# Kernel tuning notes

Hardware: AMD Instinct MI355X
Metric: run time of the kernel (lower is better)

The kernel has to match this reference:

```python
import jax, jax.numpy as jnp
import numpy as np

D_MODEL = 256
D_STATE = 16
D_CONV = 4
EXPAND = 2
D_INNER = EXPAND * D_MODEL
N = 65536


def setup_inputs() -> dict:
    key = jax.random.key(0)
    ks = jax.random.split(key, 16)
    s = lambda fan_in: 1.0 / np.sqrt(fan_in)
    inp = {
        'x': jax.random.normal(ks[0], (N, D_MODEL), jnp.float32),
        'guidance': jax.random.normal(ks[1], (N, 3), jnp.float32),
        'in_proj_w': jax.random.uniform(ks[2], (2 * D_INNER, D_MODEL), jnp.float32, -s(D_MODEL), s(D_MODEL)),
        'conv_w': jax.random.uniform(ks[3], (D_INNER, 1, D_CONV), jnp.float32, -s(D_CONV), s(D_CONV)),
        'conv_b': jax.random.uniform(ks[4], (D_INNER,), jnp.float32, -s(D_CONV), s(D_CONV)),
        'x_proj_w': jax.random.uniform(ks[5], (2 * D_STATE, D_INNER), jnp.float32, -s(D_INNER), s(D_INNER)),
        'dt_proj_w': jax.random.uniform(ks[6], (D_INNER, D_INNER), jnp.float32, -s(D_INNER), s(D_INNER)),
        'dt_proj_b': jax.random.uniform(ks[7], (D_INNER,), jnp.float32, -s(D_INNER), s(D_INNER)),
        'gg1_w': jax.random.uniform(ks[8], (D_INNER, 3), jnp.float32, -s(3), s(3)),
        'gg1_b': jax.random.uniform(ks[9], (D_INNER,), jnp.float32, -s(3), s(3)),
        'ln_g': jnp.ones((D_INNER,), jnp.float32),
        'ln_b': jnp.zeros((D_INNER,), jnp.float32),
        'gg2_w': jax.random.uniform(ks[10], (3 * D_INNER, D_INNER), jnp.float32, -s(D_INNER), s(D_INNER)),
        'gg2_b': jax.random.uniform(ks[11], (3 * D_INNER,), jnp.float32, -s(D_INNER), s(D_INNER)),
        'A_log': jnp.log(jnp.tile(jnp.arange(1, D_STATE + 1, dtype=jnp.float32), (D_INNER, 1))),
        'D': jnp.ones((D_INNER,), jnp.float32),
        'out_proj_w': jax.random.uniform(ks[12], (D_MODEL, D_INNER), jnp.float32, -s(D_INNER), s(D_INNER)),
    }
    return inp


def _layernorm(x, g, b, eps=1e-5):
    mu = jnp.mean(x, axis=-1, keepdims=True)
    var = jnp.var(x, axis=-1, keepdims=True)
    return (x - mu) * jax.lax.rsqrt(var + eps) * g + b


def _selective_scan(u, delta, A, B, C, Dp):
    # u, delta: [N, d_inner]; B, C: [N, d_state]; A: [d_inner, d_state]
    def step(h, inp):
        u_i, d_i, B_i, C_i = inp
        deltaA = jnp.exp(d_i[:, None] * A)                     # [d_inner, d_state]
        h = deltaA * h + (d_i[:, None] * B_i[None, :]) * u_i[:, None]
        y = jnp.sum(h * C_i[None, :], axis=-1) + Dp * u_i       # [d_inner]
        return h, y
    h0 = jnp.zeros((u.shape[1], A.shape[1]), u.dtype)
    _, ys = jax.lax.scan(step, h0, (u, delta, B, C))
    return ys                                                   # [N, d_inner]


def reference(x, guidance, in_proj_w, conv_w, conv_b, x_proj_w, dt_proj_w, dt_proj_b,
              gg1_w, gg1_b, ln_g, ln_b, gg2_w, gg2_b, A_log, D, out_proj_w):
    n = x.shape[0]
    xz = x @ in_proj_w.T                                        # [N, 2*d_inner]
    x_in, z = jnp.split(xz, 2, axis=-1)
    # depthwise causal conv1d over the voxel-sequence axis (pad left d_conv-1, crop to N)
    lhs = x_in.T[None]                                          # [1, d_inner, N]
    conv = jax.lax.conv_general_dilated(
        lhs, conv_w, window_strides=(1,), padding=[(D_CONV - 1, 0)],
        dimension_numbers=('NCH', 'OIH', 'NCH'), feature_group_count=D_INNER)
    x_in = conv[0].T + conv_b                                   # [N, d_inner]
    x_in = jax.nn.silu(x_in)
    # guidance gates
    g = _layernorm(guidance @ gg1_w.T + gg1_b, ln_g, ln_b)
    g = jax.nn.gelu(g, approximate=False)
    gates = g @ gg2_w.T + gg2_b                                 # [N, 3*d_inner]
    g_input, g_state, g_output = jnp.split(jax.nn.sigmoid(gates), 3, axis=-1)
    x_mod = x_in * g_input
    A = -jnp.exp(A_log)
    x_dbl = x_mod @ x_proj_w.T                                  # [N, 2*d_state]
    B, C = x_dbl[:, :D_STATE], x_dbl[:, D_STATE:]
    delta = jax.nn.softplus(x_mod @ dt_proj_w.T + dt_proj_b)
    y = _selective_scan(x_mod, delta, A, B, C, D)
    y = y * jax.nn.silu(z) * g_output
    return y @ out_proj_w.T                                     # [N, d_model]
```

## Files before the change

kernel.cpp:

```cpp
#include <hip/hip_runtime.h>
#include <math.h>

#define NTOK 65536
#define DMODEL 256
#define DI 512
#define DS 16
#define CHUNK 128
#define NCHUNK (NTOK / CHUNK)
#define QCH 128

typedef __bf16 bf16x8 __attribute__((ext_vector_type(8)));
typedef float  f32x4  __attribute__((ext_vector_type(4)));

__device__ __forceinline__ float sigf(float x) { return 1.0f / (1.0f + expf(-x)); }

__global__ __launch_bounds__(256) void wprep_kernel(
    const float* gg2_w, unsigned short* Wg)
{
    int p = blockIdx.x * 256 + threadIdx.x;
    int lg = p & 3;
    int c  = (p >> 2) & 511;
    int hl = (p >> 11) & 1;
    int kc = (p >> 12) & 15;
    int gm = p >> 16;
// ... 3 lines not shown
#pragma unroll
    for (int j = 0; j < 8; j++) {
        float x = src[j];
        __bf16 h = (__bf16)x;
        union { __bf16 b; unsigned short us; } cv;
        if (hl) cv.b = (__bf16)(x - (float)h); else cv.b = h;
        outv.u[j] = cv.us;
    }
    *(float4*)(Wg + (size_t)p * 8) = outv.f;
}

__global__ __launch_bounds__(256) void wprep_inproj(
    const float* in_proj_w, unsigned short* Wg2)
{
    int p = blockIdx.x * 256 + threadIdx.x;
    int lg = p & 3;
    int c  = (p >> 2) & 511;
    int hl = (p >> 11) & 1;
    int kc = (p >> 12) & 7;
    int gm = p >> 15;
    const float* src = in_proj_w + (size_t)(gm * 512 + c) * 256 + kc * 32 + lg * 8;
    union { unsigned short u[8]; float4 f; } outv;
#pragma unroll
    for (int j = 0; j < 8; j++) {
        float x = src[j];
        __bf16 h = (__bf16)x;
        union { __bf16 b; unsigned short us; } cv;
        if (hl) cv.b = (__bf16)(x - (float)h); else cv.b = h;
        outv.u[j] = cv.us;
    }
    *(float4*)(Wg2 + (size_t)p * 8) = outv.f;
}

__global__ __launch_bounds__(256) void wprep_dt(
    const float* dt_proj_w, unsigned short* Wdt)
{
    int p = blockIdx.x * 256 + threadIdx.x;
    int lg = p & 3;
    int c  = (p >> 2) & 127;
    int hl = (p >> 9) & 1;
    int kc = (p >> 10) & 15;
    int q  = p >> 14;
    const float* src = dt_proj_w + (size_t)(q * 128 + c) * 512 + kc * 32 + lg * 8;
    union { unsigned short u[8]; float4 f; } outv;
#pragma unroll
    for (int j = 0; j < 8; j++) {
        float x = src[j];
        __bf16 h = (__bf16)x;
        union { __bf16 b; unsigned short us; } cv;
        if (hl) cv.b = (__bf16)(x - (float)h); else cv.b = h;
        outv.u[j] = cv.us;
    }
    *(float4*)(Wdt + (size_t)p * 8) = outv.f;
}

__global__ __launch_bounds__(256) void wprep_out(
    const float* out_proj_w, unsigned short* Wout)
{
    int p = blockIdx.x * 256 + threadIdx.x;
    int lg = p & 3;
    int c  = (p >> 2) & 255;
    int hl = (p >> 10) & 1;
    int kc = p >> 11;
    const float* src = out_proj_w + (size_t)c * 512 + kc * 32 + lg * 8;
    union { unsigned short u[8]; float4 f; } outv;
#pragma unroll
    for (int j = 0; j < 8; j++) {
        float x = src[j];
        __bf16 h = (__bf16)x;
        union { __bf16 b; unsigned short us; } cv;
        if (hl) cv.b = (__bf16)(x - (float)h); else cv.b = h;
        outv.u[j] = cv.us;
    }
    *(float4*)(Wout + (size_t)p * 8) = outv.f;
}

#define MFMA_CHUNK(NFM, KC, WH, WL)                                           \
    _Pragma("unroll")                                                         \
    for (int fm = 0; fm < NFM; fm++) {                                        \
        int t = (fm < 4) ? (fm * 16 + lr) : (64 + lr);                        \
        int pidx = (t * 32 + (((KC) * 4 + lg) ^ (t & 7))) * 8;                \
        bf16x8 ah = *(const bf16x8*)&AhL[pidx];                               \
        bf16x8 al = *(const bf16x8*)&AlL[pidx];                               \
        _Pragma("unroll")                                                     \
        for (int fn = 0; fn < 4; fn++) {                                      \
            acc[fm][fn] = __builtin_amdgcn_mfma_f32_16x16x32_bf16(ah, WH[fn], acc[fm][fn], 0, 0, 0); \
            acc[fm][fn] = __builtin_amdgcn_mfma_f32_16x16x32_bf16(ah, WL[fn], acc[fm][fn], 0, 0, 0); \
            acc[fm][fn] = __builtin_amdgcn_mfma_f32_16x16x32_bf16(al, WH[fn], acc[fm][fn], 0, 0, 0); \
        }                                                                     \
    }

__global__ __launch_bounds__(512, 2) void in_conv_mfma(
    const float* x, const unsigned short* Wg2, const float* conv_w,
    const float* conv_b, float* P1, float* P2)
{
    __shared__ __align__(16) unsigned short smem[2 * 80 * 256];
    unsigned short* AhL = smem;
    unsigned short* AlL = smem + 80 * 256;
    float* xs = (float*)smem;

    const int tid = threadIdx.x;
    const int row0 = blockIdx.x * 64;
    const int l  = tid & 63;
    const int wn = tid >> 6;
    const int lr = l & 15;
    const int lg = l >> 4;
// ... 75 lines not shown
                acc[fm][fn] = (f32x4){0.f, 0.f, 0.f, 0.f};
        bf16x8 whA[4], wlA[4], whB[4], wlB[4];
        loadW(0, 0, whA, wlA);
#pragma unroll
        for (int kc = 0; kc < 8; kc += 2) {
            loadW(0, kc + 1, whB, wlB);
            MFMA_CHUNK(5, kc, whA, wlA)
            if (kc + 2 < 8) loadW(0, kc + 2, whA, wlA);
            MFMA_CHUNK(5, kc + 1, whB, wlB)
        }

        __syncthreads();
        float* xsw = xs + wn * (68 * 33);
        const int c_local = l & 31;
        const int rbase = (l >> 5) * 32;
#pragma unroll
        for (int h = 0; h < 2; h++) {
            if (h) __syncthreads();
#pragma unroll
            for (int fm = 0; fm < 5; fm++)
#pragma unroll
                for (int ff = 0; ff < 2; ff++) {
                    int fn = h * 2 + ff;
#pragma unroll
                    for (int q = 0; q < 4; q++) {
                        if (fm < 4) {
                            int rr = 4 + fm * 16 + lg * 4 + q;
                            xsw[rr * 33 + ff * 16 + lr] = acc[fm][fn][q];
                        } else if (lg == 0) {
                            xsw[q * 33 + ff * 16 + lr] = acc[fm][fn][q];
                        }
                    }
                }
            asm volatile("s_waitcnt lgkmcnt(0)" ::: "memory");
            int cg = wn * 64 + h * 32 + c_local;
            float w0 = conv_w[cg * 4 + 0], w1 = conv_w[cg * 4 + 1];
            float w2 = conv_w[cg * 4 + 2], w3 = conv_w[cg * 4 + 3];
            float cb = conv_b[cg];
            float s0 = xsw[(rbase + 1) * 33 + c_local];
            float s1 = xsw[(rbase + 2) * 33 + c_local];
            float s2 = xsw[(rbase + 3) * 33 + c_local];
#pragma unroll
            for (int i = 0; i < 32; i++) {
                float s3 = xsw[(rbase + 4 + i) * 33 + c_local];
                float cv = cb + w0 * s0 + w1 * s1 + w2 * s2 + w3 * s3;
                cv = cv * sigf(cv);
                P1[(size_t)(row0 + rbase + i) * 512 + cg] = cv;
                s0 = s1; s1 = s2; s2 = s3;
            }
        }
    }
}

__global__ __launch_bounds__(512, 2) void gates_mfma_kernel(
    const float* guidance, const float* gg1_w, const float* gg1_b,
    const float* ln_g, const float* ln_b,
    const unsigned short* Wg, const float* gg2_b,
    float* P1, float* P2)
{
    __shared__ unsigned short AhL[64 * 512];
    __shared__ unsigned short AlL[64 * 512];
    __shared__ float red_s[64][9], red_q[64][9];

    const int tid = threadIdx.x;
    const int tok = tid & 63;
    const int o   = tid >> 6;
    const int row0 = blockIdx.x * 64;

    float g0 = guidance[(size_t)(row0 + tok) * 3 + 0];
    float g1 = guidance[(size_t)(row0 + tok) * 3 + 1];
    float g2 = guidance[(size_t)(row0 + tok) * 3 + 2];
    float v[64];
    float sum = 0.f, sumsq = 0.f;
#pragma unroll
    for (int m = 0; m < 8; m++)
#pragma unroll
        for (int jj = 0; jj < 8; jj++) {
            int d = m * 64 + o * 8 + jj;
            float t = gg1_w[d * 3 + 0] * g0 + gg1_w[d * 3 + 1] * g1 +
                      gg1_w[d * 3 + 2] * g2 + gg1_b[d];
            v[m * 8 + jj] = t;
            sum += t; sumsq += t * t;
        }
    red_s[tok][o] = sum; red_q[tok][o] = sumsq;
    __syncthreads();
    sum = 0.f; sumsq = 0.f;
#pragma unroll
    for (int oo = 0; oo < 8; oo++) { sum += red_s[tok][oo]; sumsq += red_q[tok][oo]; }
    float mu = sum * (1.f / 512.f);
    float var = fmaxf(sumsq * (1.f / 512.f) - mu * mu, 0.f);
    float rstd = 1.f / sqrtf(var + 1e-5f);
#pragma unroll
    for (int m = 0; m < 8; m++) {
        bf16x8 hoct, loct;
#pragma unroll
        for (int jj = 0; jj < 8; jj++) {
            int d = m * 64 + o * 8 + jj;
            float t = (v[m * 8 + jj] - mu) * rstd * ln_g[d] + ln_b[d];
            t = 0.5f * t * (1.f + erff(t * 0.70710678118654752440f));
            __bf16 h = (__bf16)t;
            hoct[jj] = h;
            loct[jj] = (__bf16)(t - (float)h);
        }
        int pidx = ((tok * 64 + (m * 8 + o)) ^ (tok & 7)) * 8;
        *(bf16x8*)&AhL[pidx] = hoct;
        *(bf16x8*)&AlL[pidx] = loct;
    }
    __syncthreads();

    const int l  = tid & 63;
    const int wn = tid >> 6;
    const int lr = l & 15;
    const int lg = l >> 4;

    for (int gm = 0; gm < 2; gm++) {
        f32x4 acc[4][4];
#pragma unroll
        for (int fm = 0; fm < 4; fm++)
#pragma unroll
            for (int fn = 0; fn < 4; fn++)
                acc[fm][fn] = (f32x4){0.f, 0.f, 0.f, 0.f};

        bf16x8 whA[4], wlA[4], whB[4], wlB[4];

        auto loadW = [&](int kc, bf16x8 (&wh)[4], bf16x8 (&wl)[4]) {
            const unsigned short* bh = Wg + (size_t)(((gm * 16 + kc) * 2 + 0) * 2048) * 8;
            const unsigned short* bl = Wg + (size_t)(((gm * 16 + kc) * 2 + 1) * 2048) * 8;
            int pk = (wn * 64 + lr) * 4 + lg;
#pragma unroll
            for (int fn = 0; fn < 4; fn++) {
                wh[fn] = *(const bf16x8*)(bh + (size_t)(pk + fn * 64) * 8);
                wl[fn] = *(const bf16x8*)(bl + (size_t)(pk + fn * 64) * 8);
            }
        };
        auto doChunk = [&](int kc, const bf16x8 (&wh)[4], const bf16x8 (&wl)[4]) {
#pragma unroll
            for (int fm = 0; fm < 4; fm++) {
                int t = fm * 16 + lr;
                int pidx = ((t * 64 + kc * 4 + lg) ^ (lr & 7)) * 8;
                bf16x8 ah = *(const bf16x8*)&AhL[pidx];
                bf16x8 al = *(const bf16x8*)&AlL[pidx];
#pragma unroll
                for (int fn = 0; fn < 4; fn++) {
                    acc[fm][fn] = __builtin_amdgcn_mfma_f32_16x16x32_bf16(
                        ah, wh[fn], acc[fm][fn], 0, 0, 0);
                    acc[fm][fn] = __builtin_amdgcn_mfma_f32_16x16x32_bf16(
                        ah, wl[fn], acc[fm][fn], 0, 0, 0);
                    acc[fm][fn] = __builtin_amdgcn_mfma_f32_16x16x32_bf16(
                        al, wh[fn], acc[fm][fn], 0, 0, 0);
                }
            }
        };

        loadW(0, whA, wlA);
        for (int kc = 0; kc < 16; kc += 2) {
            loadW(kc + 1, whB, wlB);
            doChunk(kc, whA, wlA);
            if (kc + 2 < 16) loadW(kc + 2, whA, wlA);
            doChunk(kc + 1, whB, wlB);
        }

        float* P = gm ? P2 : P1;
        const float* bias = gg2_b + gm * 1024;
#pragma unroll
        for (int fm = 0; fm < 4; fm++)
#pragma unroll
            for (int fn = 0; fn < 4; fn++) {
                int col = wn * 64 + fn * 16 + lr;
                float b = bias[col];
#pragma unroll
                for (int q = 0; q < 4; q++) {
                    int r = row0 + fm * 16 + lg * 4 + q;
                    size_t idx = (size_t)r * 512 + col;
                    P[idx] *= sigf(acc[fm][fn][q] + b);
                }
            }
    }
}

__global__ __launch_bounds__(512, 2) void dtp_mfma(
    const float* A, const unsigned short* Wdt, const float* bias,
    int dbase, float* delta_q)
{
    __shared__ __align__(16) unsigned short AhL[64 * 512];
    __shared__ __align__(16) unsigned short AlL[64 * 512];
    const int tid = threadIdx.x;
    const int row0 = blockIdx.x * 64;

    for (int i = tid; i < 64 * 64; i += 512) {
        int t = i >> 6, k8 = i & 63;
        const float* src = A + (size_t)(row0 + t) * 512 + k8 * 8;
        float4 a0 = *(const float4*)src, a1 = *(const float4*)(src + 4);
        float xv[8] = {a0.x, a0.y, a0.z, a0.w, a1.x, a1.y, a1.z, a1.w};
        bf16x8 ho, lo;
#pragma unroll
        for (int j = 0; j < 8; j++) {
            __bf16 hh = (__bf16)xv[j];
            ho[j] = hh;
            lo[j] = (__bf16)(xv[j] - (float)hh);
        }
        int pidx = (t * 64 + (k8 ^ (t & 7))) * 8;
        *(bf16x8*)&AhL[pidx] = ho;
        *(bf16x8*)&AlL[pidx] = lo;
    }
    __syncthreads();

    const int l  = tid & 63;
    const int wv = tid >> 6;
    const int wr = wv >> 2;
    const int wc = wv & 3;
    const int lr = l & 15;
    const int lg = l >> 4;
    const unsigned short* Wq = Wdt + (size_t)(dbase >> 7) * 16384 * 8;

    f32x4 acc[2][2];
#pragma unroll
    for (int fm = 0; fm < 2; fm++)
#pragma unroll
        for (int fn = 0; fn < 2; fn++)
            acc[fm][fn] = (f32x4){0.f, 0.f, 0.f, 0.f};

    bf16x8 whA[2], wlA[2], whB[2], wlB[2];
    auto loadW = [&](int kc, bf16x8 (&wh)[2], bf16x8 (&wl)[2]) {
        const unsigned short* bh = Wq + (size_t)((kc * 2 + 0) * 512) * 8;
        const unsigned short* bl = Wq + (size_t)((kc * 2 + 1) * 512) * 8;
        int pk = (wc * 32 + lr) * 4 + lg;
#pragma unroll
        for (int fn = 0; fn < 2; fn++) {
            wh[fn] = *(const bf16x8*)(bh + (size_t)(pk + fn * 64) * 8);
            wl[fn] = *(const bf16x8*)(bl + (size_t)(pk + fn * 64) * 8);
        }
    };
    auto doChunk = [&](int kc, const bf16x8 (&wh)[2], const bf16x8 (&wl)[2]) {
#pragma unroll
        for (int fm = 0; fm < 2; fm++) {
            int t = wr * 32 + fm * 16 + lr;
            int pidx = (t * 64 + ((kc * 4 + lg) ^ (t & 7))) * 8;
            bf16x8 ah = *(const bf16x8*)&AhL[pidx];
            bf16x8 al = *(const bf16x8*)&AlL[pidx];
#pragma unroll
            for (int fn = 0; fn < 2; fn++) {
                acc[fm][fn] = __builtin_amdgcn_mfma_f32_16x16x32_bf16(
                    ah, wh[fn], acc[fm][fn], 0, 0, 0);
                acc[fm][fn] = __builtin_amdgcn_mfma_f32_16x16x32_bf16(
                    ah, wl[fn], acc[fm][fn], 0, 0, 0);
                acc[fm][fn] = __builtin_amdgcn_mfma_f32_16x16x32_bf16(
                    al, wh[fn], acc[fm][fn], 0, 0, 0);
            }
        }
    };

    loadW(0, whA, wlA);
    for (int kc = 0; kc < 16; kc += 2) {
        loadW(kc + 1, whB, wlB);
        doChunk(kc, whA, wlA);
        if (kc + 2 < 16) loadW(kc + 2, whA, wlA);
        doChunk(kc + 1, whB, wlB);
    }

#pragma unroll
    for (int fm = 0; fm < 2; fm++)
#pragma unroll
        for (int fn = 0; fn < 2; fn++) {
            int col = wc * 32 + fn * 16 + lr;
            float b = bias[dbase + col];
#pragma unroll
            for (int q = 0; q < 4; q++) {
                int r = row0 + wr * 32 + fm * 16 + lg * 4 + q;
                float s = acc[fm][fn][q] + b;
                delta_q[(size_t)r * 128 + col] =
                    fmaxf(s, 0.f) + log1pf(expf(-fabsf(s)));
            }
        }
}

__global__ __launch_bounds__(512, 2) void outp_mfma(
    const float* A, const unsigned short* Wout, float* out)
{
    __shared__ __align__(16) unsigned short AhL[64 * 512];
    __shared__ __align__(16) unsigned short AlL[64 * 512];
    const int tid = threadIdx.x;
    const int row0 = blockIdx.x * 64;

    for (int i = tid; i < 64 * 64; i += 512) {
        int t = i >> 6, k8 = i & 63;
        const float* src = A + (size_t)(row0 + t) * 512 + k8 * 8;
        float4 a0 = *(const float4*)src, a1 = *(const float4*)(src + 4);
        float xv[8] = {a0.x, a0.y, a0.z, a0.w, a1.x, a1.y, a1.z, a1.w};
        bf16x8 ho, lo;
#pragma unroll
        for (int j = 0; j < 8; j++) {
            __bf16 hh = (__bf16)xv[j];
            ho[j] = hh;
            lo[j] = (__bf16)(xv[j] - (float)hh);
        }
        int pidx = (t * 64 + (k8 ^ (t & 7))) * 8;
        *(bf16x8*)&AhL[pidx] = ho;
        *(bf16x8*)&AlL[pidx] = lo;
    }
    __syncthreads();

    const int l  = tid & 63;
    const int wv = tid >> 6;
    const int wr = wv >> 2;
    const int wc = wv & 3;
    const int lr = l & 15;
    const int lg = l >> 4;

    f32x4 acc[2][4];
#pragma unroll
    for (int fm = 0; fm < 2; fm++)
#pragma unroll
        for (int fn = 0; fn < 4; fn++)
            acc[fm][fn] = (f32x4){0.f, 0.f, 0.f, 0.f};

    bf16x8 whA[4], wlA[4], whB[4], wlB[4];
    auto loadW = [&](int kc, bf16x8 (&wh)[4], bf16x8 (&wl)[4]) {
        const unsigned short* bh = Wout + (size_t)((kc * 2 + 0) * 1024) * 8;
        const unsigned short* bl = Wout + (size_t)((kc * 2 + 1) * 1024) * 8;
        int pk = (wc * 64 + lr) * 4 + lg;
#pragma unroll
        for (int fn = 0; fn < 4; fn++) {
            wh[fn] = *(const bf16x8*)(bh + (size_t)(pk + fn * 64) * 8);
            wl[fn] = *(const bf16x8*)(bl + (size_t)(pk + fn * 64) * 8);
        }
    };
    auto doChunk = [&](int kc, const bf16x8 (&wh)[4], const bf16x8 (&wl)[4]) {
#pragma unroll
        for (int fm = 0; fm < 2; fm++) {
            int t = wr * 32 + fm * 16 + lr;
            int pidx = (t * 64 + ((kc * 4 + lg) ^ (t & 7))) * 8;
            bf16x8 ah = *(const bf16x8*)&AhL[pidx];
            bf16x8 al = *(const bf16x8*)&AlL[pidx];
#pragma unroll
            for (int fn = 0; fn < 4; fn++) {
                acc[fm][fn] = __builtin_amdgcn_mfma_f32_16x16x32_bf16(
                    ah, wh[fn], acc[fm][fn], 0, 0, 0);
                acc[fm][fn] = __builtin_amdgcn_mfma_f32_16x16x32_bf16(
                    ah, wl[fn], acc[fm][fn], 0, 0, 0);
                acc[fm][fn] = __builtin_amdgcn_mfma_f32_16x16x32_bf16(
                    al, wh[fn], acc[fm][fn], 0, 0, 0);
            }
        }
    };

    loadW(0, whA, wlA);
    for (int kc = 0; kc < 16; kc += 2) {
        loadW(kc + 1, whB, wlB);
        doChunk(kc, whA, wlA);
        if (kc + 2 < 16) loadW(kc + 2, whA, wlA);
        doChunk(kc + 1, whB, wlB);
    }

#pragma unroll
    for (int fm = 0; fm < 2; fm++)
#pragma unroll
        for (int fn = 0; fn < 4; fn++) {
            int col = wc * 64 + fn * 16 + lr;
#pragma unroll
            for (int q = 0; q < 4; q++) {
                int r = row0 + wr * 32 + fm * 16 + lg * 4 + q;
                out[(size_t)r * 256 + col] = acc[fm][fn][q];
            }
        }
}

__global__ __launch_bounds__(256) void gemm_nt32(
    const float* A, const float* W, float* out0, int K, int ldo)
{
    __shared__ float As[16][65];
    __shared__ float Ws[16][33];
    const int tid = threadIdx.x;
    const int row0 = blockIdx.x * 64;
    const int tr = (tid / 16) * 4;
    const int tc = (tid % 16) * 2;
    float acc[4][2];
#pragma unroll
    for (int i = 0; i < 4; i++) { acc[i][0] = 0.f; acc[i][1] = 0.f; }
    for (int k0 = 0; k0 < K; k0 += 16) {
        __syncthreads();
        for (int i = tid; i < 64 * 16; i += 256) {
            int m = i / 16, k = i % 16;
            As[k][m] = A[(size_t)(row0 + m) * K + k0 + k];
        }
        for (int i = tid; i < 32 * 16; i += 256) {
            int n = i / 16, k = i % 16;
            Ws[k][n] = W[(size_t)n * K + k0 + k];
        }
        __syncthreads();
#pragma unroll
        for (int kk = 0; kk < 16; kk++) {
            float a[4], b[2];
#pragma unroll
            for (int i = 0; i < 4; i++) a[i] = As[kk][tr + i];
            b[0] = Ws[kk][tc]; b[1] = Ws[kk][tc + 1];
#pragma unroll
            for (int i = 0; i < 4; i++) { acc[i][0] += a[i] * b[0]; acc[i][1] += a[i] * b[1]; }
        }
    }
#pragma unroll
    for (int i = 0; i < 4; i++) {
        int r = row0 + tr + i;
        out0[(size_t)r * ldo + tc] = acc[i][0];
        out0[(size_t)r * ldo + tc + 1] = acc[i][1];
    }
}

__global__ __launch_bounds__(256) void scan_pass1(
    const float* delta_q, const float* u_full, const float* xdbl,
    const float* A_log, int dbase, float* h_end, float* Ssum)
{
    int c = blockIdx.x;
    int tid = threadIdx.x;
    int dl = tid >> 1;
    int sh = (tid & 1) * 8;
    int d = dbase + dl;
    float As[8];
#pragma unroll
    for (int s = 0; s < 8; s++) As[s] = -expf(A_log[d * 16 + sh + s]);
    float h[8];
#pragma unroll
    for (int s = 0; s < 8; s++) h[s] = 0.f;
    float S = 0.f;
    __shared__ float Bs[CHUNK][17];
    int tbase = c * CHUNK;
    for (int i = tid; i < CHUNK * 16; i += 256) {
        int r = i >> 4, s = i & 15;
        Bs[r][s] = xdbl[(size_t)(tbase + r) * 32 + s];
    }
    __syncthreads();
    for (int tl = 0; tl < CHUNK; tl++) {
        size_t t = (size_t)tbase + tl;
        float de = delta_q[t * QCH + dl];
        float uu = u_full[t * DI + d];
        float du = de * uu;
        S += de;
#pragma unroll
        for (int s = 0; s < 8; s++)
            h[s] = __expf(de * As[s]) * h[s] + du * Bs[tl][sh + s];
    }
    size_t base = ((size_t)c * QCH + dl) * 16 + sh;
#pragma unroll
    for (int s = 0; s < 8; s++) h_end[base + s] = h[s];
    if ((tid & 1) == 0) Ssum[(size_t)c * QCH + dl] = S;
}

#define GRP 16
#define NGRP (NCHUNK / GRP)

__global__ __launch_bounds__(256) void scan_pass2a(
    const float* h_end, const float* Ssum, const float* A_log, int dbase,
    float* Pagg, float* Hagg)
{
    int idx = blockIdx.x * 256 + threadIdx.x;
    int g = blockIdx.y;
    int dl = idx >> 4;
    float As = -expf(A_log[(dbase + dl) * 16 + (idx & 15)]);
    float P = 1.f, H = 0.f;
// ... 65 lines not shown
        float de = delta_q[t * QCH + dl];
        float uu = u_full[t * DI + d];
        float du = de * uu;
        float y = 0.f;
#pragma unroll
        for (int s = 0; s < 8; s++) {
            h[s] = __expf(de * As[s]) * h[s] + du * Bs[tl][sh + s];
            y += h[s] * Cs[tl][sh + s];
        }
        y += __shfl_xor(y, 1);
        if ((tid & 1) == 0)
            wg_ymod[t * DI + d] = (y + Dd * uu) * wg_ymod[t * DI + d];
    }
}

extern "C" void kernel_launch(void* const* d_in, const int* in_sizes, int n_in,
                              void* d_out, int out_size, void* d_ws, size_t ws_size,
                              hipStream_t stream)
{
    const float* x         = (const float*)d_in[0];
    const float* guidance  = (const float*)d_in[1];
    const float* in_proj_w = (const float*)d_in[2];
    const float* conv_w    = (const float*)d_in[3];
    const float* conv_b    = (const float*)d_in[4];
    const float* x_proj_w  = (const float*)d_in[5];
    const float* dt_proj_w = (const float*)d_in[6];
    const float* dt_proj_b = (const float*)d_in[7];
    const float* gg1_w     = (const float*)d_in[8];
    const float* gg1_b     = (const float*)d_in[9];
    const float* ln_g      = (const float*)d_in[10];
    const float* ln_b      = (const float*)d_in[11];
    const float* gg2_w     = (const float*)d_in[12];
    const float* gg2_b     = (const float*)d_in[13];
    const float* A_log     = (const float*)d_in[14];
    const float* Dp        = (const float*)d_in[15];
    const float* out_proj_w= (const float*)d_in[16];
    float* out = (float*)d_out;

    float* P1 = (float*)d_ws;
    float* P2 = P1 + (size_t)NTOK * DI;

    float* ob      = (float*)d_out;
    float* delta_q = ob;
    float* xdbl    = ob + (size_t)NTOK * QCH;
    float* h_end   = ob + (size_t)NTOK * (QCH + 32);
    float* Ssum    = h_end + (size_t)NCHUNK * QCH * DS;
    float* initS   = Ssum + (size_t)NCHUNK * QCH;
    unsigned short* Wg  = (unsigned short*)(initS + (size_t)NCHUNK * QCH * DS);
    unsigned short* Wg2 = Wg  + (size_t)131072 * 8;
    unsigned short* Wdt = Wg2 + (size_t)65536 * 8;
    float* Pagg  = (float*)(Wdt + (size_t)65536 * 8);
    float* Hagg  = Pagg + NGRP * 2048;
    float* Ginit = Hagg + NGRP * 2048;
    unsigned short* Wout = (unsigned short*)P1;

    wprep_kernel<<<512, 256, 0, stream>>>(gg2_w, Wg);
    wprep_inproj<<<256, 256, 0, stream>>>(in_proj_w, Wg2);
    wprep_dt<<<256, 256, 0, stream>>>(dt_proj_w, Wdt);
    in_conv_mfma<<<NTOK / 64, 512, 0, stream>>>(
        x, Wg2, conv_w, conv_b, P1, P2);
    gates_mfma_kernel<<<NTOK / 64, 512, 0, stream>>>(
        guidance, gg1_w, gg1_b, ln_g, ln_b, Wg, gg2_b, P1, P2);
    gemm_nt32<<<NTOK / 64, 256, 0, stream>>>(P1, x_proj_w, xdbl, DI, 32);
    for (int q = 0; q < 4; q++) {
        int dbase = q * QCH;
        dtp_mfma<<<NTOK / 64, 512, 0, stream>>>(
            P1, Wdt, dt_proj_b, dbase, delta_q);
        scan_pass1<<<NCHUNK, 256, 0, stream>>>(
            delta_q, P1, xdbl, A_log, dbase, h_end, Ssum);
        scan_pass2a<<<dim3(8, NGRP), 256, 0, stream>>>(
            h_end, Ssum, A_log, dbase, Pagg, Hagg);
        scan_pass2b<<<8, 256, 0, stream>>>(Pagg, Hagg, Ginit);
        scan_pass2c<<<dim3(8, NGRP), 256, 0, stream>>>(
            h_end, Ssum, A_log, dbase, Ginit, initS);
        scan_pass3<<<NCHUNK, 256, 0, stream>>>(
            delta_q, P1, xdbl, A_log, dbase, initS, Dp, P2);
    }
    wprep_out<<<128, 256, 0, stream>>>(out_proj_w, Wout);
    outp_mfma<<<NTOK / 64, 512, 0, stream>>>(P2, Wout, out);
}
```

Baseline: 1.795 ms.

## Halve LDS tiles via K-split staging and raise occupancy in MFMA GEMM kernels

The gates, dt-proj and out-proj MFMA kernels now stage the split-bf16 activation tile in two K halves of 256, halving shared memory per block, and launch bounds go from 2 to 4 blocks per CU. The gates kernel also moves its two output groups onto a second grid dimension instead of looping, and recomputes the LayerNorm input instead of holding 64 values in registers. The weight-load double buffering is dropped in favour of plain per-chunk loads, leaning on the higher occupancy to hide latency. The costs are an extra barrier per block, duplicated LayerNorm/GELU work in the gates kernel, and tighter register limits that could cause spills.

```diff
diff --git a/kernel.cpp b/kernel.cpp
--- a/kernel.cpp
+++ b/kernel.cpp
@@ -260,25 +260,25 @@
     }
 }
 
-__global__ __launch_bounds__(512, 2) void gates_mfma_kernel(
+__global__ __launch_bounds__(512, 4) void gates_mfma_kernel(
     const float* guidance, const float* gg1_w, const float* gg1_b,
     const float* ln_g, const float* ln_b,
     const unsigned short* Wg, const float* gg2_b,
     float* P1, float* P2)
 {
-    __shared__ unsigned short AhL[64 * 512];
-    __shared__ unsigned short AlL[64 * 512];
+    __shared__ __align__(16) unsigned short AhL[64 * 256];
+    __shared__ __align__(16) unsigned short AlL[64 * 256];
     __shared__ float red_s[64][9], red_q[64][9];
 
     const int tid = threadIdx.x;
     const int tok = tid & 63;
     const int o   = tid >> 6;
     const int row0 = blockIdx.x * 64;
+    const int gm  = blockIdx.y;
 
     float g0 = guidance[(size_t)(row0 + tok) * 3 + 0];
     float g1 = guidance[(size_t)(row0 + tok) * 3 + 1];
     float g2 = guidance[(size_t)(row0 + tok) * 3 + 2];
-    float v[64];
     float sum = 0.f, sumsq = 0.f;
 #pragma unroll
     for (int m = 0; m < 8; m++)
@@ -287,7 +287,6 @@
             int d = m * 64 + o * 8 + jj;
             float t = gg1_w[d * 3 + 0] * g0 + gg1_w[d * 3 + 1] * g1 +
                       gg1_w[d * 3 + 2] * g2 + gg1_b[d];
-            v[m * 8 + jj] = t;
             sum += t; sumsq += t * t;
         }
     red_s[tok][o] = sum; red_q[tok][o] = sumsq;
@@ -298,54 +297,59 @@
     float mu = sum * (1.f / 512.f);
     float var = fmaxf(sumsq * (1.f / 512.f) - mu * mu, 0.f);
     float rstd = 1.f / sqrtf(var + 1e-5f);
-#pragma unroll
-    for (int m = 0; m < 8; m++) {
-        bf16x8 hoct, loct;
-#pragma unroll
-        for (int jj = 0; jj < 8; jj++) {
-            int d = m * 64 + o * 8 + jj;
-            float t = (v[m * 8 + jj] - mu) * rstd * ln_g[d] + ln_b[d];
-            t = 0.5f * t * (1.f + erff(t * 0.70710678118654752440f));
-            __bf16 h = (__bf16)t;
-            hoct[jj] = h;
-            loct[jj] = (__bf16)(t - (float)h);
-        }
-        int pidx = ((tok * 64 + (m * 8 + o)) ^ (tok & 7)) * 8;
-        *(bf16x8*)&AhL[pidx] = hoct;
-        *(bf16x8*)&AlL[pidx] = loct;
-    }
-    __syncthreads();
 
     const int l  = tid & 63;
     const int wn = tid >> 6;
     const int lr = l & 15;
     const int lg = l >> 4;
 
-    for (int gm = 0; gm < 2; gm++) {
-        f32x4 acc[4][4];
-#pragma unroll
-        for (int fm = 0; fm < 4; fm++)
-#pragma unroll
-            for (int fn = 0; fn < 4; fn++)
-                acc[fm][fn] = (f32x4){0.f, 0.f, 0.f, 0.f};
-
-        bf16x8 whA[4], wlA[4], whB[4], wlB[4];
-
-        auto loadW = [&](int kc, bf16x8 (&wh)[4], bf16x8 (&wl)[4]) {
-            const unsigned short* bh = Wg + (size_t)(((gm * 16 + kc) * 2 + 0) * 2048) * 8;
-            const unsigned short* bl = Wg + (size_t)(((gm * 16 + kc) * 2 + 1) * 2048) * 8;
-            int pk = (wn * 64 + lr) * 4 + lg;
-#pragma unroll
-            for (int fn = 0; fn < 4; fn++) {
-                wh[fn] = *(const bf16x8*)(bh + (size_t)(pk + fn * 64) * 8);
-                wl[fn] = *(const bf16x8*)(bl + (size_t)(pk + fn * 64) * 8);
-            }
-        };
-        auto doChunk = [&](int kc, const bf16x8 (&wh)[4], const bf16x8 (&wl)[4]) {
+    f32x4 acc[4][4];
+#pragma unroll
+    for (int fm = 0; fm < 4; fm++)
+#pragma unroll
+        for (int fn = 0; fn < 4; fn++)
+            acc[fm][fn] = (f32x4){0.f, 0.f, 0.f, 0.f};
+
+    for (int kh = 0; kh < 2; kh++) {
+        __syncthreads();
+#pragma unroll
+        for (int mm = 0; mm < 4; mm++) {
+            int m = kh * 4 + mm;
+            bf16x8 hoct, loct;
+#pragma unroll
+            for (int jj = 0; jj < 8; jj++) {
+                int d = m * 64 + o * 8 + jj;
+                float t = gg1_w[d * 3 + 0] * g0 + gg1_w[d * 3 + 1] * g1 +
+                          gg1_w[d * 3 + 2] * g2 + gg1_b[d];
+                t = (t - mu) * rstd * ln_g[d] + ln_b[d];
+                t = 0.5f * t * (1.f + erff(t * 0.70710678118654752440f));
+                __bf16 h = (__bf16)t;
+                hoct[jj] = h;
+                loct[jj] = (__bf16)(t - (float)h);
+            }
+            int k8l = mm * 8 + o;
+            int pidx = (tok * 32 + (k8l ^ (tok & 7))) * 8;
+            *(bf16x8*)&AhL[pidx] = hoct;
+            *(bf16x8*)&AlL[pidx] = loct;
+        }
+        __syncthreads();
+        for (int kc = 0; kc < 8; kc++) {
+            bf16x8 wh[4], wl[4];
+            {
+                int kcg = kh * 8 + kc;
+                const unsigned short* bh = Wg + (size_t)(((gm * 16 + kcg) * 2 + 0) * 2048) * 8;
+                const unsigned short* bl = Wg + (size_t)(((gm * 16 + kcg) * 2 + 1) * 2048) * 8;
+                int pk = (wn * 64 + lr) * 4 + lg;
+#pragma unroll
+                for (int fn = 0; fn < 4; fn++) {
+                    wh[fn] = *(const bf16x8*)(bh + (size_t)(pk + fn * 64) * 8);
+                    wl[fn] = *(const bf16x8*)(bl + (size_t)(pk + fn * 64) * 8);
+                }
+            }
 #pragma unroll
             for (int fm = 0; fm < 4; fm++) {
                 int t = fm * 16 + lr;
-                int pidx = ((t * 64 + kc * 4 + lg) ^ (lr & 7)) * 8;
+                int pidx = (t * 32 + ((kc * 4 + lg) ^ (t & 7))) * 8;
                 bf16x8 ah = *(const bf16x8*)&AhL[pidx];
                 bf16x8 al = *(const bf16x8*)&AlL[pidx];
 #pragma unroll
@@ -358,60 +362,34 @@
                         al, wh[fn], acc[fm][fn], 0, 0, 0);
                 }
             }
-        };
-
-        loadW(0, whA, wlA);
-        for (int kc = 0; kc < 16; kc += 2) {
-            loadW(kc + 1, whB, wlB);
-            doChunk(kc, whA, wlA);
-            if (kc + 2 < 16) loadW(kc + 2, whA, wlA);
-            doChunk(kc + 1, whB, wlB);
-        }
-
-        float* P = gm ? P2 : P1;
-        const float* bias = gg2_b + gm * 1024;
-#pragma unroll
-        for (int fm = 0; fm < 4; fm++)
-#pragma unroll
-            for (int fn = 0; fn < 4; fn++) {
-                int col = wn * 64 + fn * 16 + lr;
-                float b = bias[col];
-#pragma unroll
-                for (int q = 0; q < 4; q++) {
-                    int r = row0 + fm * 16 + lg * 4 + q;
-                    size_t idx = (size_t)r * 512 + col;
-                    P[idx] *= sigf(acc[fm][fn][q] + b);
-                }
-            }
-    }
-}
-
-__global__ __launch_bounds__(512, 2) void dtp_mfma(
+        }
+    }
+
+    float* P = gm ? P2 : P1;
+    const float* bias = gg2_b + gm * 1024;
+#pragma unroll
+    for (int fm = 0; fm < 4; fm++)
+#pragma unroll
+        for (int fn = 0; fn < 4; fn++) {
+            int col = wn * 64 + fn * 16 + lr;
+            float b = bias[col];
+#pragma unroll
+            for (int q = 0; q < 4; q++) {
+                int r = row0 + fm * 16 + lg * 4 + q;
+                size_t idx = (size_t)r * 512 + col;
+                P[idx] *= sigf(acc[fm][fn][q] + b);
+            }
+        }
+}
+
+__global__ __launch_bounds__(512, 4) void dtp_mfma(
     const float* A, const unsigned short* Wdt, const float* bias,
     int dbase, float* delta_q)
 {
-    __shared__ __align__(16) unsigned short AhL[64 * 512];
-    __shared__ __align__(16) unsigned short AlL[64 * 512];
+    __shared__ __align__(16) unsigned short AhL[64 * 256];
+    __shared__ __align__(16) unsigned short AlL[64 * 256];
     const int tid = threadIdx.x;
     const int row0 = blockIdx.x * 64;
-
-    for (int i = tid; i < 64 * 64; i += 512) {
-        int t = i >> 6, k8 = i & 63;
-        const float* src = A + (size_t)(row0 + t) * 512 + k8 * 8;
-        float4 a0 = *(const float4*)src, a1 = *(const float4*)(src + 4);
-        float xv[8] = {a0.x, a0.y, a0.z, a0.w, a1.x, a1.y, a1.z, a1.w};
-        bf16x8 ho, lo;
-#pragma unroll
-        for (int j = 0; j < 8; j++) {
-            __bf16 hh = (__bf16)xv[j];
-            ho[j] = hh;
-            lo[j] = (__bf16)(xv[j] - (float)hh);
-        }
-        int pidx = (t * 64 + (k8 ^ (t & 7))) * 8;
-        *(bf16x8*)&AhL[pidx] = ho;
-        *(bf16x8*)&AlL[pidx] = lo;
-    }
-    __syncthreads();
 
     const int l  = tid & 63;
     const int wv = tid >> 6;
@@ -428,42 +406,55 @@
         for (int fn = 0; fn < 2; fn++)
             acc[fm][fn] = (f32x4){0.f, 0.f, 0.f, 0.f};
 
-    bf16x8 whA[2], wlA[2], whB[2], wlB[2];
-    auto loadW = [&](int kc, bf16x8 (&wh)[2], bf16x8 (&wl)[2]) {
-        const unsigned short* bh = Wq + (size_t)((kc * 2 + 0) * 512) * 8;
-        const unsigned short* bl = Wq + (size_t)((kc * 2 + 1) * 512) * 8;
-        int pk = (wc * 32 + lr) * 4 + lg;
-#pragma unroll
-        for (int fn = 0; fn < 2; fn++) {
-            wh[fn] = *(const bf16x8*)(bh + (size_t)(pk + fn * 64) * 8);
-            wl[fn] = *(const bf16x8*)(bl + (size_t)(pk + fn * 64) * 8);
-        }
-    };
-    auto doChunk = [&](int kc, const bf16x8 (&wh)[2], const bf16x8 (&wl)[2]) {
-#pragma unroll
-        for (int fm = 0; fm < 2; fm++) {
-            int t = wr * 32 + fm * 16 + lr;
-            int pidx = (t * 64 + ((kc * 4 + lg) ^ (t & 7))) * 8;
-            bf16x8 ah = *(const bf16x8*)&AhL[pidx];
-            bf16x8 al = *(const bf16x8*)&AlL[pidx];
-#pragma unroll
-            for (int fn = 0; fn < 2; fn++) {
-                acc[fm][fn] = __builtin_amdgcn_mfma_f32_16x16x32_bf16(
-                    ah, wh[fn], acc[fm][fn], 0, 0, 0);
-                acc[fm][fn] = __builtin_amdgcn_mfma_f32_16x16x32_bf16(
-                    ah, wl[fn], acc[fm][fn], 0, 0, 0);
-                acc[fm][fn] = __builtin_amdgcn_mfma_f32_16x16x32_bf16(
-                    al, wh[fn], acc[fm][fn], 0, 0, 0);
-            }
-        }
-    };
-
-    loadW(0, whA, wlA);
-    for (int kc = 0; kc < 16; kc += 2) {
-        loadW(kc + 1, whB, wlB);
-        doChunk(kc, whA, wlA);
-        if (kc + 2 < 16) loadW(kc + 2, whA, wlA);
-        doChunk(kc + 1, whB, wlB);
+    for (int kh = 0; kh < 2; kh++) {
+        if (kh) __syncthreads();
+        for (int i = tid; i < 64 * 32; i += 512) {
+            int t = i >> 5, k8 = i & 31;
+            const float* src = A + (size_t)(row0 + t) * 512 + kh * 256 + k8 * 8;
+            float4 a0 = *(const float4*)src, a1 = *(const float4*)(src + 4);
+            float xv[8] = {a0.x, a0.y, a0.z, a0.w, a1.x, a1.y, a1.z, a1.w};
+            bf16x8 ho, lo;
+#pragma unroll
+            for (int j = 0; j < 8; j++) {
+                __bf16 hh = (__bf16)xv[j];
+                ho[j] = hh;
+                lo[j] = (__bf16)(xv[j] - (float)hh);
+            }
+            int pidx = (t * 32 + (k8 ^ (t & 7))) * 8;
+            *(bf16x8*)&AhL[pidx] = ho;
+            *(bf16x8*)&AlL[pidx] = lo;
+        }
+        __syncthreads();
+        for (int kc = 0; kc < 8; kc++) {
+            bf16x8 wh[2], wl[2];
+            {
+                int kcg = kh * 8 + kc;
+                const unsigned short* bh = Wq + (size_t)((kcg * 2 + 0) * 512) * 8;
+                const unsigned short* bl = Wq + (size_t)((kcg * 2 + 1) * 512) * 8;
+                int pk = (wc * 32 + lr) * 4 + lg;
+#pragma unroll
+                for (int fn = 0; fn < 2; fn++) {
+                    wh[fn] = *(const bf16x8*)(bh + (size_t)(pk + fn * 64) * 8);
+                    wl[fn] = *(const bf16x8*)(bl + (size_t)(pk + fn * 64) * 8);
+                }
+            }
+#pragma unroll
+            for (int fm = 0; fm < 2; fm++) {
+                int t = wr * 32 + fm * 16 + lr;
+                int pidx = (t * 32 + ((kc * 4 + lg) ^ (t & 7))) * 8;
+                bf16x8 ah = *(const bf16x8*)&AhL[pidx];
+                bf16x8 al = *(const bf16x8*)&AlL[pidx];
+#pragma unroll
+                for (int fn = 0; fn < 2; fn++) {
+                    acc[fm][fn] = __builtin_amdgcn_mfma_f32_16x16x32_bf16(
+                        ah, wh[fn], acc[fm][fn], 0, 0, 0);
+                    acc[fm][fn] = __builtin_amdgcn_mfma_f32_16x16x32_bf16(
+                        ah, wl[fn], acc[fm][fn], 0, 0, 0);
+                    acc[fm][fn] = __builtin_amdgcn_mfma_f32_16x16x32_bf16(
+                        al, wh[fn], acc[fm][fn], 0, 0, 0);
+                }
+            }
+        }
     }
 
 #pragma unroll
@@ -482,31 +473,13 @@
         }
 }
 
-__global__ __launch_bounds__(512, 2) void outp_mfma(
+__global__ __launch_bounds__(512, 4) void outp_mfma(
     const float* A, const unsigned short* Wout, float* out)
 {
-    __shared__ __align__(16) unsigned short AhL[64 * 512];
-    __shared__ __align__(16) unsigned short AlL[64 * 512];
+    __shared__ __align__(16) unsigned short AhL[64 * 256];
+    __shared__ __align__(16) unsigned short AlL[64 * 256];
     const int tid = threadIdx.x;
     const int row0 = blockIdx.x * 64;
-
-    for (int i = tid; i < 64 * 64; i += 512) {
-        int t = i >> 6, k8 = i & 63;
-        const float* src = A + (size_t)(row0 + t) * 512 + k8 * 8;
-        float4 a0 = *(const float4*)src, a1 = *(const float4*)(src + 4);
-        float xv[8] = {a0.x, a0.y, a0.z, a0.w, a1.x, a1.y, a1.z, a1.w};
-        bf16x8 ho, lo;
-#pragma unroll
-        for (int j = 0; j < 8; j++) {
-            __bf16 hh = (__bf16)xv[j];
-            ho[j] = hh;
-            lo[j] = (__bf16)(xv[j] - (float)hh);
-        }
-        int pidx = (t * 64 + (k8 ^ (t & 7))) * 8;
-        *(bf16x8*)&AhL[pidx] = ho;
-        *(bf16x8*)&AlL[pidx] = lo;
-    }
-    __syncthreads();
 
     const int l  = tid & 63;
     const int wv = tid >> 6;
@@ -522,42 +495,55 @@
         for (int fn = 0; fn < 4; fn++)
             acc[fm][fn] = (f32x4){0.f, 0.f, 0.f, 0.f};
 
-    bf16x8 whA[4], wlA[4], whB[4], wlB[4];
-    auto loadW = [&](int kc, bf16x8 (&wh)[4], bf16x8 (&wl)[4]) {
-        const unsigned short* bh = Wout + (size_t)((kc * 2 + 0) * 1024) * 8;
-        const unsigned short* bl = Wout + (size_t)((kc * 2 + 1) * 1024) * 8;
-        int pk = (wc * 64 + lr) * 4 + lg;
-#pragma unroll
-        for (int fn = 0; fn < 4; fn++) {
-            wh[fn] = *(const bf16x8*)(bh + (size_t)(pk + fn * 64) * 8);
-            wl[fn] = *(const bf16x8*)(bl + (size_t)(pk + fn * 64) * 8);
-        }
-    };
-    auto doChunk = [&](int kc, const bf16x8 (&wh)[4], const bf16x8 (&wl)[4]) {
-#pragma unroll
-        for (int fm = 0; fm < 2; fm++) {
-            int t = wr * 32 + fm * 16 + lr;
-            int pidx = (t * 64 + ((kc * 4 + lg) ^ (t & 7))) * 8;
-            bf16x8 ah = *(const bf16x8*)&AhL[pidx];
-            bf16x8 al = *(const bf16x8*)&AlL[pidx];
-#pragma unroll
-            for (int fn = 0; fn < 4; fn++) {
-                acc[fm][fn] = __builtin_amdgcn_mfma_f32_16x16x32_bf16(
-                    ah, wh[fn], acc[fm][fn], 0, 0, 0);
-                acc[fm][fn] = __builtin_amdgcn_mfma_f32_16x16x32_bf16(
-                    ah, wl[fn], acc[fm][fn], 0, 0, 0);
-                acc[fm][fn] = __builtin_amdgcn_mfma_f32_16x16x32_bf16(
-                    al, wh[fn], acc[fm][fn], 0, 0, 0);
-            }
-        }
-    };
-
-    loadW(0, whA, wlA);
-    for (int kc = 0; kc < 16; kc += 2) {
-        loadW(kc + 1, whB, wlB);
-        doChunk(kc, whA, wlA);
-        if (kc + 2 < 16) loadW(kc + 2, whA, wlA);
-        doChunk(kc + 1, whB, wlB);
+    for (int kh = 0; kh < 2; kh++) {
+        if (kh) __syncthreads();
+        for (int i = tid; i < 64 * 32; i += 512) {
+            int t = i >> 5, k8 = i & 31;
+            const float* src = A + (size_t)(row0 + t) * 512 + kh * 256 + k8 * 8;
+            float4 a0 = *(const float4*)src, a1 = *(const float4*)(src + 4);
+            float xv[8] = {a0.x, a0.y, a0.z, a0.w, a1.x, a1.y, a1.z, a1.w};
+            bf16x8 ho, lo;
+#pragma unroll
+            for (int j = 0; j < 8; j++) {
+                __bf16 hh = (__bf16)xv[j];
+                ho[j] = hh;
+                lo[j] = (__bf16)(xv[j] - (float)hh);
+            }
+            int pidx = (t * 32 + (k8 ^ (t & 7))) * 8;
+            *(bf16x8*)&AhL[pidx] = ho;
+            *(bf16x8*)&AlL[pidx] = lo;
+        }
+        __syncthreads();
+        for (int kc = 0; kc < 8; kc++) {
+            bf16x8 wh[4], wl[4];
+            {
+                int kcg = kh * 8 + kc;
+                const unsigned short* bh = Wout + (size_t)((kcg * 2 + 0) * 1024) * 8;
+                const unsigned short* bl = Wout + (size_t)((kcg * 2 + 1) * 1024) * 8;
+                int pk = (wc * 64 + lr) * 4 + lg;
+#pragma unroll
+                for (int fn = 0; fn < 4; fn++) {
+                    wh[fn] = *(const bf16x8*)(bh + (size_t)(pk + fn * 64) * 8);
+                    wl[fn] = *(const bf16x8*)(bl + (size_t)(pk + fn * 64) * 8);
+                }
+            }
+#pragma unroll
+            for (int fm = 0; fm < 2; fm++) {
+                int t = wr * 32 + fm * 16 + lr;
+                int pidx = (t * 32 + ((kc * 4 + lg) ^ (t & 7))) * 8;
+                bf16x8 ah = *(const bf16x8*)&AhL[pidx];
+                bf16x8 al = *(const bf16x8*)&AlL[pidx];
+#pragma unroll
+                for (int fn = 0; fn < 4; fn++) {
+                    acc[fm][fn] = __builtin_amdgcn_mfma_f32_16x16x32_bf16(
+                        ah, wh[fn], acc[fm][fn], 0, 0, 0);
+                    acc[fm][fn] = __builtin_amdgcn_mfma_f32_16x16x32_bf16(
+                        ah, wl[fn], acc[fm][fn], 0, 0, 0);
+                    acc[fm][fn] = __builtin_amdgcn_mfma_f32_16x16x32_bf16(
+                        al, wh[fn], acc[fm][fn], 0, 0, 0);
+                }
+            }
+        }
     }
 
 #pragma unroll
@@ -790,7 +776,7 @@
     wprep_dt<<<256, 256, 0, stream>>>(dt_proj_w, Wdt);
     in_conv_mfma<<<NTOK / 64, 512, 0, stream>>>(
         x, Wg2, conv_w, conv_b, P1, P2);
-    gates_mfma_kernel<<<NTOK / 64, 512, 0, stream>>>(
+    gates_mfma_kernel<<<dim3(NTOK / 64, 2), 512, 0, stream>>>(
         guidance, gg1_w, gg1_b, ln_g, ln_b, Wg, gg2_b, P1, P2);
     gemm_nt32<<<NTOK / 64, 256, 0, stream>>>(P1, x_proj_w, xdbl, DI, 32);
     for (int q = 0; q < 4; q++) {
```

Result: slower. 1.922 ms (+7.1%).

## Fuse x_proj GEMM into first dt_proj MFMA pass and triple-buffer gate weights

Applied to the files above, without the earlier changes.

Removes the separate FP32 SIMT gemm_nt32 kernel for x_proj. Its weights are now pre-split into bf16 hi/lo and the product is computed with MFMA inside the first dt_proj kernel launch, reusing the A tiles already staged in shared memory. Only waves with wc<2 do the extra MFMAs, which adds some imbalance within that launch. Separately, the gates kernel now keeps three register buffers of weight chunks in a fully unrolled loop, which raises register pressure.

```diff
diff --git a/kernel.cpp b/kernel.cpp
--- a/kernel.cpp
+++ b/kernel.cpp
@@ -79,6 +79,27 @@
         outv.u[j] = cv.us;
     }
     *(float4*)(Wdt + (size_t)p * 8) = outv.f;
+}
+
+__global__ __launch_bounds__(256) void wprep_xp(
+    const float* x_proj_w, unsigned short* Wxp)
+{
+    int p = blockIdx.x * 256 + threadIdx.x;
+    int lg = p & 3;
+    int c  = (p >> 2) & 31;
+    int hl = (p >> 7) & 1;
+    int kc = p >> 8;
+    const float* src = x_proj_w + (size_t)c * 512 + kc * 32 + lg * 8;
+    union { unsigned short u[8]; float4 f; } outv;
+#pragma unroll
+    for (int j = 0; j < 8; j++) {
+        float x = src[j];
+        __bf16 h = (__bf16)x;
+        union { __bf16 b; unsigned short us; } cv;
+        if (hl) cv.b = (__bf16)(x - (float)h); else cv.b = h;
+        outv.u[j] = cv.us;
+    }
+    *(float4*)(Wxp + (size_t)p * 8) = outv.f;
 }
 
 __global__ __launch_bounds__(256) void wprep_out(
@@ -329,7 +350,7 @@
             for (int fn = 0; fn < 4; fn++)
                 acc[fm][fn] = (f32x4){0.f, 0.f, 0.f, 0.f};
 
-        bf16x8 whA[4], wlA[4], whB[4], wlB[4];
+        bf16x8 whB3[3][4], wlB3[3][4];
 
         auto loadW = [&](int kc, bf16x8 (&wh)[4], bf16x8 (&wl)[4]) {
             const unsigned short* bh = Wg + (size_t)(((gm * 16 + kc) * 2 + 0) * 2048) * 8;
@@ -360,12 +381,12 @@
             }
         };
 
-        loadW(0, whA, wlA);
-        for (int kc = 0; kc < 16; kc += 2) {
-            loadW(kc + 1, whB, wlB);
-            doChunk(kc, whA, wlA);
-            if (kc + 2 < 16) loadW(kc + 2, whA, wlA);
-            doChunk(kc + 1, whB, wlB);
+        loadW(0, whB3[0], wlB3[0]);
+        loadW(1, whB3[1], wlB3[1]);
+#pragma unroll
+        for (int i = 0; i < 16; i++) {
+            if (i + 2 < 16) loadW(i + 2, whB3[(i + 2) % 3], wlB3[(i + 2) % 3]);
+            doChunk(i, whB3[i % 3], wlB3[i % 3]);
         }
 
         float* P = gm ? P2 : P1;
@@ -386,9 +407,10 @@
     }
 }
 
+template <bool XP>
 __global__ __launch_bounds__(512, 2) void dtp_mfma(
-    const float* A, const unsigned short* Wdt, const float* bias,
-    int dbase, float* delta_q)
+    const float* A, const unsigned short* Wdt, const unsigned short* Wxp,
+    const float* bias, int dbase, float* delta_q, float* xdbl)
 {
     __shared__ __align__(16) unsigned short AhL[64 * 512];
     __shared__ __align__(16) unsigned short AlL[64 * 512];
@@ -420,6 +442,7 @@
     const int lr = l & 15;
     const int lg = l >> 4;
     const unsigned short* Wq = Wdt + (size_t)(dbase >> 7) * 16384 * 8;
+    const bool doXP = XP && (wc < 2);
 
     f32x4 acc[2][2];
 #pragma unroll
@@ -427,9 +450,14 @@
 #pragma unroll
         for (int fn = 0; fn < 2; fn++)
             acc[fm][fn] = (f32x4){0.f, 0.f, 0.f, 0.f};
+    f32x4 axp[2];
+    axp[0] = (f32x4){0.f, 0.f, 0.f, 0.f};
+    axp[1] = (f32x4){0.f, 0.f, 0.f, 0.f};
 
     bf16x8 whA[2], wlA[2], whB[2], wlB[2];
-    auto loadW = [&](int kc, bf16x8 (&wh)[2], bf16x8 (&wl)[2]) {
+    bf16x8 xwA, xlA, xwB, xlB;
+    auto loadW = [&](int kc, bf16x8 (&wh)[2], bf16x8 (&wl)[2],
+                     bf16x8& xw, bf16x8& xl) {
         const unsigned short* bh = Wq + (size_t)((kc * 2 + 0) * 512) * 8;
         const unsigned short* bl = Wq + (size_t)((kc * 2 + 1) * 512) * 8;
         int pk = (wc * 32 + lr) * 4 + lg;
@@ -438,8 +466,16 @@
             wh[fn] = *(const bf16x8*)(bh + (size_t)(pk + fn * 64) * 8);
             wl[fn] = *(const bf16x8*)(bl + (size_t)(pk + fn * 64) * 8);
         }
+        if (doXP) {
+            const unsigned short* xh = Wxp + (size_t)((kc * 2 + 0) * 128) * 8;
+            const unsigned short* xlo = Wxp + (size_t)((kc * 2 + 1) * 128) * 8;
+            int pkx = (wc * 16 + lr) * 4 + lg;
+            xw = *(const bf16x8*)(xh + (size_t)pkx * 8);
+            xl = *(const bf16x8*)(xlo + (size_t)pkx * 8);
+        }
     };
-    auto doChunk = [&](int kc, const bf16x8 (&wh)[2], const bf16x8 (&wl)[2]) {
+    auto doChunk = [&](int kc, const bf16x8 (&wh)[2], const bf16x8 (&wl)[2],
+                       const bf16x8& xw, const bf16x8& xl) {
 #pragma unroll
         for (int fm = 0; fm < 2; fm++) {
             int t = wr * 32 + fm * 16 + lr;
@@ -455,15 +491,23 @@
                 acc[fm][fn] = __builtin_amdgcn_mfma_f32_16x16x32_bf16(
                     al, wh[fn], acc[fm][fn], 0, 0, 0);
             }
+            if (doXP) {
+                axp[fm] = __builtin_amdgcn_mfma_f32_16x16x32_bf16(
+                    ah, xw, axp[fm], 0, 0, 0);
+                axp[fm] = __builtin_amdgcn_mfma_f32_16x16x32_bf16(
+                    ah, xl, axp[fm], 0, 0, 0);
+                axp[fm] = __builtin_amdgcn_mfma_f32_16x16x32_bf16(
+                    al, xw, axp[fm], 0, 0, 0);
+            }
         }
     };
 
-    loadW(0, whA, wlA);
+    loadW(0, whA, wlA, xwA, xlA);
     for (int kc = 0; kc < 16; kc += 2) {
-        loadW(kc + 1, whB, wlB);
-        doChunk(kc, whA, wlA);
-        if (kc + 2 < 16) loadW(kc + 2, whA, wlA);
-        doChunk(kc + 1, whB, wlB);
+        loadW(kc + 1, whB, wlB, xwB, xlB);
+        doChunk(kc, whA, wlA, xwA, xlA);
+        if (kc + 2 < 16) loadW(kc + 2, whA, wlA, xwA, xlA);
+        doChunk(kc + 1, whB, wlB, xwB, xlB);
     }
 
 #pragma unroll
@@ -480,6 +524,17 @@
                     fmaxf(s, 0.f) + log1pf(expf(-fabsf(s)));
             }
         }
+    if (doXP) {
+#pragma unroll
+        for (int fm = 0; fm < 2; fm++) {
+            int col = wc * 16 + lr;
+#pragma unroll
+            for (int q = 0; q < 4; q++) {
+                int r = row0 + wr * 32 + fm * 16 + lg * 4 + q;
+                xdbl[(size_t)r * 32 + col] = axp[fm][q];
+            }
+        }
+    }
 }
 
 __global__ __launch_bounds__(512, 2) void outp_mfma(
@@ -571,47 +626,6 @@
                 out[(size_t)r * 256 + col] = acc[fm][fn][q];
             }
         }
-}
-
-__global__ __launch_bounds__(256) void gemm_nt32(
-    const float* A, const float* W, float* out0, int K, int ldo)
-{
-    __shared__ float As[16][65];
-    __shared__ float Ws[16][33];
-    const int tid = threadIdx.x;
-    const int row0 = blockIdx.x * 64;
-    const int tr = (tid / 16) * 4;
-    const int tc = (tid % 16) * 2;
-    float acc[4][2];
-#pragma unroll
-    for (int i = 0; i < 4; i++) { acc[i][0] = 0.f; acc[i][1] = 0.f; }
-    for (int k0 = 0; k0 < K; k0 += 16) {
-        __syncthreads();
-        for (int i = tid; i < 64 * 16; i += 256) {
-            int m = i / 16, k = i % 16;
-            As[k][m] = A[(size_t)(row0 + m) * K + k0 + k];
-        }
-        for (int i = tid; i < 32 * 16; i += 256) {
-            int n = i / 16, k = i % 16;
-            Ws[k][n] = W[(size_t)n * K + k0 + k];
-        }
-        __syncthreads();
-#pragma unroll
-        for (int kk = 0; kk < 16; kk++) {
-            float a[4], b[2];
-#pragma unroll
-            for (int i = 0; i < 4; i++) a[i] = As[kk][tr + i];
-            b[0] = Ws[kk][tc]; b[1] = Ws[kk][tc + 1];
-#pragma unroll
-            for (int i = 0; i < 4; i++) { acc[i][0] += a[i] * b[0]; acc[i][1] += a[i] * b[1]; }
-        }
-    }
-#pragma unroll
-    for (int i = 0; i < 4; i++) {
-        int r = row0 + tr + i;
-        out0[(size_t)r * ldo + tc] = acc[i][0];
-        out0[(size_t)r * ldo + tc + 1] = acc[i][1];
-    }
 }
 
 __global__ __launch_bounds__(256) void scan_pass1(
@@ -783,20 +797,25 @@
     float* Pagg  = (float*)(Wdt + (size_t)65536 * 8);
     float* Hagg  = Pagg + NGRP * 2048;
     float* Ginit = Hagg + NGRP * 2048;
+    unsigned short* Wxp = (unsigned short*)(Ginit + NGRP * 2048);
     unsigned short* Wout = (unsigned short*)P1;
 
     wprep_kernel<<<512, 256, 0, stream>>>(gg2_w, Wg);
     wprep_inproj<<<256, 256, 0, stream>>>(in_proj_w, Wg2);
     wprep_dt<<<256, 256, 0, stream>>>(dt_proj_w, Wdt);
+    wprep_xp<<<16, 256, 0, stream>>>(x_proj_w, Wxp);
     in_conv_mfma<<<NTOK / 64, 512, 0, stream>>>(
         x, Wg2, conv_w, conv_b, P1, P2);
     gates_mfma_kernel<<<NTOK / 64, 512, 0, stream>>>(
         guidance, gg1_w, gg1_b, ln_g, ln_b, Wg, gg2_b, P1, P2);
-    gemm_nt32<<<NTOK / 64, 256, 0, stream>>>(P1, x_proj_w, xdbl, DI, 32);
     for (int q = 0; q < 4; q++) {
         int dbase = q * QCH;
-        dtp_mfma<<<NTOK / 64, 512, 0, stream>>>(
-            P1, Wdt, dt_proj_b, dbase, delta_q);
+        if (q == 0)
+            dtp_mfma<true><<<NTOK / 64, 512, 0, stream>>>(
+                P1, Wdt, Wxp, dt_proj_b, dbase, delta_q, xdbl);
+        else
+            dtp_mfma<false><<<NTOK / 64, 512, 0, stream>>>(
+                P1, Wdt, nullptr, dt_proj_b, dbase, delta_q, xdbl);
         scan_pass1<<<NCHUNK, 256, 0, stream>>>(
             delta_q, P1, xdbl, A_log, dbase, h_end, Ssum);
         scan_pass2a<<<dim3(8, NGRP), 256, 0, stream>>>(
```

Result: slower. 2.404 ms (+33.9%).
